# Optimization experiments

Measured on AMD Instinct MI355X. Metric: run time of the kernel, lower is better.

The kernel has to match this reference:

```python
import jax, jax.numpy as jnp
import numpy as np

B, S, D = 8, 2048, 512
H, DK, DV = 8, 64, 64


def setup_inputs() -> dict:
    key = jax.random.key(0)
    ks = jax.random.split(key, 12)
    def xavier(k, shape):
        fan_in, fan_out = shape[0], shape[1]
        std = (2.0 / (fan_in + fan_out)) ** 0.5
        return jax.random.normal(k, shape, dtype=jnp.float32) * std
    return {
        "Q": jax.random.normal(ks[0], (B, S, D), dtype=jnp.float32),
        "K": jax.random.normal(ks[1], (B, S, D), dtype=jnp.float32),
        "V": jax.random.normal(ks[2], (B, S, D), dtype=jnp.float32),
        "W_q": xavier(ks[3], (D, H * DK)),
        "W_k": xavier(ks[4], (D, H * DK)),
        "W_v": xavier(ks[5], (D, H * DV)),
        "W_o": xavier(ks[6], (H * DV, D)),
        "W1": xavier(ks[7], (D, D)),  # linear1.weight, stored [out, in]
        "b1": jnp.zeros((D,), dtype=jnp.float32),
        "W2": xavier(ks[8], (D, D)),  # linear2.weight
        "b2": jnp.zeros((D,), dtype=jnp.float32),
    }


def reference(Q, K, V, W_q, W_k, W_v, W_o, W1, b1, W2, b2):
    eps = 1e-6
    bsz, q_len, _ = Q.shape
    # project and split heads: [B, S, H, dk]
    Qh = (Q @ W_q).reshape(bsz, q_len, H, DK)
    Kh = (K @ W_k).reshape(bsz, q_len, H, DK)
    Vh = (V @ W_v).reshape(bsz, q_len, H, DV)
    temperature = DK ** 0.5
    # scores: [B, H, Sq, Sk] (full O(N^2) matrix, as in original)
    scores = jnp.einsum('bqhd,bkhd->bhqk', Qh, Kh) / (temperature + eps)
    probs = jax.nn.softmax(scores, axis=-1)  # dropout = identity (eval)
    V_att = jnp.einsum('bhqk,bkhd->bqhd', probs, Vh).reshape(bsz, q_len, H * DV)
    attn_out = V_att @ W_o  # dropout = identity
    X = Q + attn_out
    # FFN: linear2(relu(linear1(X))); torch Linear: x @ W.T + b
    ffn = jax.nn.relu(X @ W1.T + b1) @ W2.T + b2
    return ffn + X
```

## Files before the change

kernel.cpp:

```cpp
#include <hip/hip_runtime.h>
#include <stdint.h>

typedef __bf16 bf16;
typedef bf16 bf16x8 __attribute__((ext_vector_type(8)));
typedef bf16 bf16x4 __attribute__((ext_vector_type(4)));
typedef float f32x2 __attribute__((ext_vector_type(2)));
typedef float f32x4 __attribute__((ext_vector_type(4)));
typedef float f32x16 __attribute__((ext_vector_type(16)));

#define AS1 __attribute__((address_space(1)))
#define AS3 __attribute__((address_space(3)))

__device__ __forceinline__ void gll16(const void* g, void* l) {
    __builtin_amdgcn_global_load_lds((const AS1 unsigned int*)g,
                                     (AS3 unsigned int*)l, 16, 0, 0);
}

__device__ __forceinline__ bf16 f2bf(float x) { return (bf16)x; }

__device__ __forceinline__ float fexp2(float x) { return __builtin_amdgcn_exp2f(x); }

#define QSCALE_LOG2E 0.18033685757f

__global__ void k_castqkv(const float* __restrict__ Q, const float* __restrict__ K,
                          const float* __restrict__ V,
                          bf16* __restrict__ oq, bf16* __restrict__ ok, bf16* __restrict__ ov)
{
    const int z = blockIdx.y;
    const float* in = z == 0 ? Q : z == 1 ? K : V;
    bf16* out = z == 0 ? oq : z == 1 ? ok : ov;
    const int i = blockIdx.x * 256 + threadIdx.x;
    for (size_t j = (size_t)i * 4; j < 8388608u; j += (size_t)2048 * 256 * 4) {
        float4 v = *(const float4*)(in + j);
        bf16x4 o;
        o[0] = f2bf(v.x); o[1] = f2bf(v.y); o[2] = f2bf(v.z); o[3] = f2bf(v.w);
        *(bf16x4*)(out + j) = o;
    }
}

__global__ void k_castw(const float* __restrict__ Wq, const float* __restrict__ Wk,
                        const float* __restrict__ Wv, const float* __restrict__ Wo,
                        const float* __restrict__ W1, const float* __restrict__ W2,
                        bf16* __restrict__ oq, bf16* __restrict__ ok, bf16* __restrict__ ov,
                        bf16* __restrict__ oo, bf16* __restrict__ o1, bf16* __restrict__ o2)
{
    const int z = blockIdx.y;
    const int idx = blockIdx.x * 256 + threadIdx.x;
    const float* src = z == 0 ? Wq : z == 1 ? Wk : z == 2 ? Wv : z == 3 ? Wo : z == 4 ? W1 : W2;
    bf16* dst = z == 0 ? oq : z == 1 ? ok : z == 2 ? ov : z == 3 ? oo : z == 4 ? o1 : o2;
    if (z < 4) {
        const int n = idx >> 9, k = idx & 511;
        dst[idx] = f2bf(src[(k << 9) + n]);
    } else {
        dst[idx] = f2bf(src[idx]);
    }
}

__device__ __forceinline__ void gemm_core(const bf16* __restrict__ A,
                                          const bf16* __restrict__ Bt,
                                          const int K, bf16* As, bf16* Bs,
                                          const int bm, const int bn,
                                          f32x4 acc[4][4])
{
    const int tid  = threadIdx.x;
    const int lane = tid & 63;
    const int wave = tid >> 6;
    const int g    = lane >> 4;
    const int l15  = lane & 15;
    const int wm   = (wave >> 1) * 64;
    const int wn   = (wave & 1) * 64;

    const int srow = tid >> 2;
    const int sk   = (tid & 3) * 8;
    const size_t aoff0 = (size_t)(bm + srow) * K + sk;
    const size_t aoff1 = (size_t)(bm + 64 + srow) * K + sk;
    const size_t boff0 = (size_t)(bn + srow) * K + sk;
    const size_t boff1 = (size_t)(bn + 64 + srow) * K + sk;
    char* asb = (char*)As + wave * 1024;
    char* bsb = (char*)Bs + wave * 1024;

    for (int kt = 0; kt < K; kt += 32) {
        __syncthreads();
        gll16(A + aoff0 + kt, asb);
        gll16(A + aoff1 + kt, asb + 4096);
        gll16(Bt + boff0 + kt, bsb);
        gll16(Bt + boff1 + kt, bsb + 4096);
        __syncthreads();
        bf16x8 af[4], bfv[4];
#pragma unroll
        for (int mi = 0; mi < 4; ++mi)
            af[mi] = *(const bf16x8*)&As[(wm + mi * 16 + l15) * 32 + g * 8];
#pragma unroll
        for (int ni = 0; ni < 4; ++ni)
            bfv[ni] = *(const bf16x8*)&Bs[(wn + ni * 16 + l15) * 32 + g * 8];
#pragma unroll
        for (int mi = 0; mi < 4; ++mi)
#pragma unroll
            for (int ni = 0; ni < 4; ++ni)
                acc[mi][ni] = __builtin_amdgcn_mfma_f32_16x16x32_bf16(
                    af[mi], bfv[ni], acc[mi][ni], 0, 0, 0);
    }
}

template<int EPI>
__global__ __launch_bounds__(256)
void k_gemm(const bf16* __restrict__ A, const bf16* __restrict__ Bt,
            const float* __restrict__ bias,
            const bf16* __restrict__ residb,
            float* __restrict__ Cf, bf16* __restrict__ Cb,
            int M, int N, int K)
{
    __shared__ bf16 As[128 * 32];
    __shared__ bf16 Bs[128 * 32];
    const int bm = blockIdx.y * 128, bn = blockIdx.x * 128;
    f32x4 acc[4][4] = {};
    gemm_core(A, Bt, K, As, Bs, bm, bn, acc);

    const int tid  = threadIdx.x;
    const int lane = tid & 63;
    const int wave = tid >> 6;
    const int g    = lane >> 4;
    const int l15  = lane & 15;
    const int wm   = (wave >> 1) * 64;
    const int wn   = (wave & 1) * 64;
    const int col0 = bn + wn + l15;
#pragma unroll
    for (int ni = 0; ni < 4; ++ni) {
        const int col = col0 + ni * 16;
        float bv = 0.f;
        if constexpr (EPI == 2 || EPI == 3) bv = bias[col];
#pragma unroll
        for (int mi = 0; mi < 4; ++mi) {
#pragma unroll
            for (int r = 0; r < 4; ++r) {
                const int row = bm + wm + mi * 16 + 4 * g + r;
                const size_t idx = (size_t)row * N + col;
                float v = acc[mi][ni][r];
                if constexpr (EPI == 1) {
                    Cb[idx] = f2bf(v + (float)residb[idx]);
                } else if constexpr (EPI == 2) {
                    Cb[idx] = f2bf(fmaxf(v + bv, 0.f));
                } else {
                    Cf[idx] = v + bv + (float)residb[idx];
                }
            }
        }
    }
}

__global__ __launch_bounds__(256)
void k_proj(const bf16* __restrict__ Qb, const bf16* __restrict__ Kb, const bf16* __restrict__ Vb,
            const bf16* __restrict__ BQ, const bf16* __restrict__ BK, const bf16* __restrict__ BV,
            bf16* __restrict__ OQ, bf16* __restrict__ OK_, bf16* __restrict__ OV)
{
    __shared__ bf16 SM[8192];
    const int z = blockIdx.z;
    const bf16* A  = z == 0 ? Qb : z == 1 ? Kb : Vb;
    const bf16* Bt = z == 0 ? BQ : z == 1 ? BK : BV;
    bf16* Cb       = z == 0 ? OQ : z == 1 ? OK_ : OV;
    const int bm = blockIdx.y * 128, bn = blockIdx.x * 128;
    f32x4 acc[4][4] = {};
    gemm_core(A, Bt, 512, SM, SM + 4096, bm, bn, acc);

    const int tid  = threadIdx.x;
    const int lane = tid & 63;
    const int wave = tid >> 6;
    const int g    = lane >> 4;
    const int l15  = lane & 15;
    const int wn   = (wave & 1) * 64;
    const int bb   = bm >> 11;
    const int s0   = bm & 2047;

    __syncthreads();
#pragma unroll
    for (int p = 0; p < 2; ++p) {
        if ((wave >> 1) == p) {
            if (z == 0) {
#pragma unroll
                for (int ni = 0; ni < 4; ++ni) {
                    const int col = wn + ni * 16 + l15;
                    const int hh = col >> 6, dk = col & 63;
                    char* img = (char*)SM + hh * 8192;
#pragma unroll
                    for (int mi = 0; mi < 4; ++mi)
#pragma unroll
                        for (int r = 0; r < 4; ++r) {
                            const int sl = mi * 16 + 4 * g + r;
                            *(bf16*)(img + (sl * 64 + dk) * 2) =
                                f2bf(acc[mi][ni][r] * QSCALE_LOG2E);
                        }
                }
            } else if (z == 1) {
#pragma unroll
                for (int ni = 0; ni < 4; ++ni) {
                    const int col = wn + ni * 16 + l15;
                    const int hh = col >> 6, dk = col & 63;
                    const int ks = dk >> 4, h2 = (dk >> 3) & 1, e = dk & 7;
                    char* img = (char*)SM + hh * 8192;
#pragma unroll
                    for (int mi = 0; mi < 4; ++mi)
#pragma unroll
                        for (int r = 0; r < 4; ++r) {
                            const int sl = mi * 16 + 4 * g + r;
                            const int t2 = sl >> 5, ql = sl & 31;
                            const int off = (((t2 * 4 + ks) * 64 + h2 * 32 + ql) * 8 + e) * 2;
                            *(bf16*)(img + off) = f2bf(acc[mi][ni][r]);
                        }
                }
            } else {
#pragma unroll
                for (int ni = 0; ni < 4; ++ni) {
                    const int col = wn + ni * 16 + l15;
                    const int hh = col >> 6, dv = col & 63;
                    const int dvt = dv >> 5, ql = dv & 31;
                    char* img = (char*)SM + hh * 8192;
#pragma unroll
                    for (int mi = 0; mi < 4; ++mi)
#pragma unroll
                        for (int r = 0; r < 4; ++r) {
                            const int sl = mi * 16 + 4 * g + r;
                            const int kt = sl >> 4, kk = sl & 15;
                            const int h2 = (kk >> 2) & 1;
                            const int e = (kk & 3) | ((kk >> 3) << 2);
                            const int off = (((dvt * 4 + kt) * 64 + h2 * 32 + ql) * 8 + e) * 2;
                            *(bf16*)(img + off) = f2bf(acc[mi][ni][r]);
                        }
                }
            }
        }
        __syncthreads();
        {
            const int hh = tid >> 7, t = tid & 127;
            const int hg = (bn >> 6) + hh;
            const size_t a0 = (size_t)(bb * 8 + hg) * 131072;
            const size_t slab = (z == 0) ? a0 + (size_t)(s0 + p * 64) * 64
                                         : a0 + (size_t)((s0 >> 6) + p) * 4096;
            const char* img = (const char*)SM + hh * 8192;
#pragma unroll
            for (int i = 0; i < 4; ++i) {
                const int G = i * 128 + t;
                bf16x8 vv = *(const bf16x8*)(img + G * 16);
                *(bf16x8*)&Cb[slab + (size_t)G * 8] = vv;
            }
        }
        if (p == 0) __syncthreads();
    }
}

__global__ __launch_bounds__(256, 2)
void k_attn(const bf16* __restrict__ Qp, const bf16* __restrict__ Khp,
            const bf16* __restrict__ Vtp, bf16* __restrict__ O)
{
    __shared__ bf16 smem[16384];
    const int tid = threadIdx.x;
    const int l   = tid & 63;
    const int w   = tid >> 6;
    const int h   = l >> 5;
    const int ql  = l & 31;
    const int d   = blockIdx.x;
    const int bh  = ((d >> 6) << 3) | (d & 7);
    const int qt  = (d >> 3) & 7;
    const size_t base = (size_t)bh * 131072;
    const int q0 = qt * 256 + w * 64;
    const int loff = l * 16;

    bf16x8 qfA[4], qfB[4];
#pragma unroll
    for (int ks = 0; ks < 4; ++ks) {
        qfA[ks] = *(const bf16x8*)&Qp[base + (size_t)(q0 + ql) * 64 + ks * 16 + h * 8];
        qfB[ks] = *(const bf16x8*)&Qp[base + (size_t)(q0 + 32 + ql) * 64 + ks * 16 + h * 8];
    }

    f32x16 oA0 = {}, oA1 = {}, oB0 = {}, oB1 = {};
    float lrunA = 0.f, lrunB = 0.f;

    const bf16* ksrc = Khp + base + tid * 8;
    const bf16* vsrc = Vtp + base + tid * 8;
    char* kb0 = (char*)smem;
    char* kb1 = (char*)smem + 16384;
    const int wdst = w * 1024;

    auto stage = [&](int kvt, char* kb) {
        const bf16* ks = ksrc + kvt * 4096;
        const bf16* vs = vsrc + kvt * 4096;
        gll16(ks,        kb + wdst);
        gll16(ks + 2048, kb + 4096 + wdst);
        gll16(vs,        kb + 8192 + wdst);
        gll16(vs + 2048, kb + 12288 + wdst);
    };

    auto compute = [&](const char* kb) {
        f32x16 sA0 = {}, sA1 = {}, sB0 = {}, sB1 = {};
        __builtin_amdgcn_s_setprio(1);
#pragma unroll
        for (int ks = 0; ks < 4; ++ks) {
            bf16x8 a0 = *(const bf16x8*)(kb + ks * 1024 + loff);
            bf16x8 a1 = *(const bf16x8*)(kb + 4096 + ks * 1024 + loff);
            sA0 = __builtin_amdgcn_mfma_f32_32x32x16_bf16(a0, qfA[ks], sA0, 0, 0, 0);
            sB0 = __builtin_amdgcn_mfma_f32_32x32x16_bf16(a0, qfB[ks], sB0, 0, 0, 0);
            sA1 = __builtin_amdgcn_mfma_f32_32x32x16_bf16(a1, qfA[ks], sA1, 0, 0, 0);
            sB1 = __builtin_amdgcn_mfma_f32_32x32x16_bf16(a1, qfB[ks], sB1, 0, 0, 0);
        }
        __builtin_amdgcn_s_setprio(0);

        f32x2 pA = {0.f, 0.f}, pB = {0.f, 0.f};
#pragma unroll
        for (int r = 0; r < 16; r += 2) {
            sA0[r]     = fexp2(sA0[r]);
            sA0[r + 1] = fexp2(sA0[r + 1]);
            sA1[r]     = fexp2(sA1[r]);
            sA1[r + 1] = fexp2(sA1[r + 1]);
            pA += (f32x2){sA0[r], sA0[r + 1]};
            pA += (f32x2){sA1[r], sA1[r + 1]};
        }
#pragma unroll
        for (int r = 0; r < 16; r += 2) {
            sB0[r]     = fexp2(sB0[r]);
            sB0[r + 1] = fexp2(sB0[r + 1]);
            sB1[r]     = fexp2(sB1[r]);
            sB1[r + 1] = fexp2(sB1[r + 1]);
            pB += (f32x2){sB0[r], sB0[r + 1]};
            pB += (f32x2){sB1[r], sB1[r + 1]};
        }
        lrunA += pA[0] + pA[1];
        lrunB += pB[0] + pB[1];

        bf16x8 pbA[4], pbB[4];
#pragma unroll
        for (int j = 0; j < 4; ++j) {
            const int ofs = 8 * (j & 1);
#pragma unroll
            for (int e = 0; e < 8; ++e) {
                pbA[j][e] = f2bf((j & 2) ? sA1[ofs + e] : sA0[ofs + e]);
                pbB[j][e] = f2bf((j & 2) ? sB1[ofs + e] : sB0[ofs + e]);
            }
        }

        const char* vr = kb + 8192;
        __builtin_amdgcn_s_setprio(1);
#pragma unroll
        for (int j = 0; j < 4; ++j) {
            bf16x8 a0 = *(const bf16x8*)(vr + j * 1024 + loff);
            bf16x8 a1 = *(const bf16x8*)(vr + 4096 + j * 1024 + loff);
            oA0 = __builtin_amdgcn_mfma_f32_32x32x16_bf16(a0, pbA[j], oA0, 0, 0, 0);
            oB0 = __builtin_amdgcn_mfma_f32_32x32x16_bf16(a0, pbB[j], oB0, 0, 0, 0);
            oA1 = __builtin_amdgcn_mfma_f32_32x32x16_bf16(a1, pbA[j], oA1, 0, 0, 0);
            oB1 = __builtin_amdgcn_mfma_f32_32x32x16_bf16(a1, pbB[j], oB1, 0, 0, 0);
        }
        __builtin_amdgcn_s_setprio(0);
    };

    stage(0, kb0);
    __syncthreads();
    for (int kvt = 0; kvt < 32; kvt += 2) {
        if (kvt + 1 < 32) stage(kvt + 1, kb1);
        compute(kb0);
        __syncthreads();
        if (kvt + 2 < 32) stage(kvt + 2, kb0);
        compute(kb1);
        __syncthreads();
    }

    char* ot = (char*)smem + w * 4096;
    const int qr = l >> 1;
    const int dh4 = (l & 1) * 4;
    auto epi = [&](const f32x16& e0, const f32x16& e1, float lr, int qg) {
        lr += __shfl_xor(lr, 32);
        const float inv = 1.f / lr;
#pragma unroll
        for (int dvt = 0; dvt < 2; ++dvt) {
#pragma unroll
            for (int r = 0; r < 16; ++r) {
                const int dv = dvt * 32 + (r & 3) + 8 * (r >> 2) + 4 * h;
                const float val = (dvt ? e1[r] : e0[r]) * inv;
                *(bf16*)(ot + ql * 128 + ((((dv >> 3) ^ (ql & 7)) << 4) | ((dv & 7) << 1))) = f2bf(val);
            }
        }
        const size_t ob = ((size_t)(bh >> 3) * 2048 + qg + qr) * 512 + (bh & 7) * 64 + (size_t)dh4 * 8;
#pragma unroll
        for (int B = 0; B < 4; ++B) {
            bf16x8 v = *(const bf16x8*)(ot + qr * 128 + (((dh4 + B) ^ (qr & 7)) << 4));
            *(bf16x8*)&O[ob + B * 8] = v;
        }
    };
    epi(oA0, oA1, lrunA, q0);
    epi(oB0, oB1, lrunB, q0 + 32);
}

extern "C" void kernel_launch(void* const* d_in, const int* in_sizes, int n_in,
                              void* d_out, int out_size, void* d_ws, size_t ws_size,
                              hipStream_t stream)
{
    const float* Q  = (const float*)d_in[0];
    const float* K  = (const float*)d_in[1];
    const float* V  = (const float*)d_in[2];
    const float* Wq = (const float*)d_in[3];
    const float* Wk = (const float*)d_in[4];
    const float* Wv = (const float*)d_in[5];
    const float* Wo = (const float*)d_in[6];
    const float* W1 = (const float*)d_in[7];
    const float* b1 = (const float*)d_in[8];
    const float* W2 = (const float*)d_in[9];
    const float* b2 = (const float*)d_in[10];
    float* out = (float*)d_out;

    const int M = 8 * 2048;
    const size_t TN = (size_t)M * 512;
    const int WN = 512 * 512;

    char* ws = (char*)d_ws;
    bf16* Qbf  = (bf16*)ws;
    bf16* Kbf  = Qbf + TN;
    bf16* Vbf  = Kbf + TN;
    bf16* Qhp  = Vbf + TN;
    bf16* Khp  = Qhp + TN;
    bf16* Vtp  = Khp + TN;
    bf16* Vatt = Vtp + TN;
    bf16* H1   = Vatt + TN;
    bf16* Wqt  = H1 + TN;
    bf16* Wkt  = Wqt + WN;
    bf16* Wvt  = Wkt + WN;
    bf16* Wot  = Wvt + WN;
    bf16* W1b  = Wot + WN;
    bf16* W2b  = W1b + WN;
    bf16* Xbf  = Vbf;

    k_castqkv<<<dim3(2048, 3), 256, 0, stream>>>(Q, K, V, Qbf, Kbf, Vbf);
    k_castw<<<dim3(1024, 6), 256, 0, stream>>>(Wq, Wk, Wv, Wo, W1, W2,
                                               Wqt, Wkt, Wvt, Wot, W1b, W2b);

    k_proj<<<dim3(4, 128, 3), 256, 0, stream>>>(Qbf, Kbf, Vbf, Wqt, Wkt, Wvt,
                                                Qhp, Khp, Vtp);

    k_attn<<<512, 256, 0, stream>>>(Qhp, Khp, Vtp, Vatt);

    dim3 gg(4, 128);
    k_gemm<1><<<gg, 256, 0, stream>>>(Vatt, Wot, nullptr, Qbf, nullptr, Xbf, M, 512, 512);
    k_gemm<2><<<gg, 256, 0, stream>>>(Xbf, W1b, b1, nullptr, nullptr, H1, M, 512, 512);
    k_gemm<3><<<gg, 256, 0, stream>>>(H1, W2b, b2, Xbf, out, nullptr, M, 512, 512);
}
```

Baseline: 210.2 us.

## Drop pre-tiled QKV projection layouts; attention reads natural row-major and transposed V

The projection kernel no longer stages its output through LDS into MFMA-ready tiled images. It writes Q and K row-major (Q pre-scaled) and V transposed per head directly from registers. The attention kernel now gathers K and V tiles from these natural layouts, using an XOR swizzle on the V staging and split 8-byte LDS reads. The residual for the first output GEMM now comes from the fp32 Q input instead of its bf16 copy, which also changes accuracy slightly. This removes the projection epilogue's LDS round trip and barriers, at the cost of strided scalar/4-wide global stores and less contiguous attention loads.

```diff
diff --git a/kernel.cpp b/kernel.cpp
--- a/kernel.cpp
+++ b/kernel.cpp
@@ -105,7 +105,7 @@
 template<int EPI>
 __global__ __launch_bounds__(256)
 void k_gemm(const bf16* __restrict__ A, const bf16* __restrict__ Bt,
-            const float* __restrict__ bias,
+            const float* __restrict__ bias, const float* __restrict__ residf,
             const bf16* __restrict__ residb,
             float* __restrict__ Cf, bf16* __restrict__ Cb,
             int M, int N, int K)
@@ -137,7 +137,7 @@
                 const size_t idx = (size_t)row * N + col;
                 float v = acc[mi][ni][r];
                 if constexpr (EPI == 1) {
-                    Cb[idx] = f2bf(v + (float)residb[idx]);
+                    Cb[idx] = f2bf(v + residf[idx]);
                 } else if constexpr (EPI == 2) {
                     Cb[idx] = f2bf(fmaxf(v + bv, 0.f));
                 } else {
@@ -153,103 +153,55 @@
             const bf16* __restrict__ BQ, const bf16* __restrict__ BK, const bf16* __restrict__ BV,
             bf16* __restrict__ OQ, bf16* __restrict__ OK_, bf16* __restrict__ OV)
 {
-    __shared__ bf16 SM[8192];
+    __shared__ bf16 As[128 * 32];
+    __shared__ bf16 Bs[128 * 32];
     const int z = blockIdx.z;
     const bf16* A  = z == 0 ? Qb : z == 1 ? Kb : Vb;
     const bf16* Bt = z == 0 ? BQ : z == 1 ? BK : BV;
     bf16* Cb       = z == 0 ? OQ : z == 1 ? OK_ : OV;
     const int bm = blockIdx.y * 128, bn = blockIdx.x * 128;
     f32x4 acc[4][4] = {};
-    gemm_core(A, Bt, 512, SM, SM + 4096, bm, bn, acc);
+    gemm_core(A, Bt, 512, As, Bs, bm, bn, acc);
 
     const int tid  = threadIdx.x;
     const int lane = tid & 63;
     const int wave = tid >> 6;
     const int g    = lane >> 4;
     const int l15  = lane & 15;
+    const int wm   = (wave >> 1) * 64;
     const int wn   = (wave & 1) * 64;
-    const int bb   = bm >> 11;
-    const int s0   = bm & 2047;
-
-    __syncthreads();
-#pragma unroll
-    for (int p = 0; p < 2; ++p) {
-        if ((wave >> 1) == p) {
-            if (z == 0) {
-#pragma unroll
-                for (int ni = 0; ni < 4; ++ni) {
-                    const int col = wn + ni * 16 + l15;
-                    const int hh = col >> 6, dk = col & 63;
-                    char* img = (char*)SM + hh * 8192;
-#pragma unroll
-                    for (int mi = 0; mi < 4; ++mi)
-#pragma unroll
-                        for (int r = 0; r < 4; ++r) {
-                            const int sl = mi * 16 + 4 * g + r;
-                            *(bf16*)(img + (sl * 64 + dk) * 2) =
-                                f2bf(acc[mi][ni][r] * QSCALE_LOG2E);
-                        }
+    const int col0 = bn + wn + l15;
+#pragma unroll
+    for (int ni = 0; ni < 4; ++ni) {
+        const int col = col0 + ni * 16;
+        if (z < 2) {
+            const float sc = (z == 0) ? QSCALE_LOG2E : 1.f;
+#pragma unroll
+            for (int mi = 0; mi < 4; ++mi)
+#pragma unroll
+                for (int r = 0; r < 4; ++r) {
+                    const int row = bm + wm + mi * 16 + 4 * g + r;
+                    Cb[(size_t)row * 512 + col] = f2bf(acc[mi][ni][r] * sc);
                 }
-            } else if (z == 1) {
-#pragma unroll
-                for (int ni = 0; ni < 4; ++ni) {
-                    const int col = wn + ni * 16 + l15;
-                    const int hh = col >> 6, dk = col & 63;
-                    const int ks = dk >> 4, h2 = (dk >> 3) & 1, e = dk & 7;
-                    char* img = (char*)SM + hh * 8192;
-#pragma unroll
-                    for (int mi = 0; mi < 4; ++mi)
-#pragma unroll
-                        for (int r = 0; r < 4; ++r) {
-                            const int sl = mi * 16 + 4 * g + r;
-                            const int t2 = sl >> 5, ql = sl & 31;
-                            const int off = (((t2 * 4 + ks) * 64 + h2 * 32 + ql) * 8 + e) * 2;
-                            *(bf16*)(img + off) = f2bf(acc[mi][ni][r]);
-                        }
-                }
-            } else {
-#pragma unroll
-                for (int ni = 0; ni < 4; ++ni) {
-                    const int col = wn + ni * 16 + l15;
-                    const int hh = col >> 6, dv = col & 63;
-                    const int dvt = dv >> 5, ql = dv & 31;
-                    char* img = (char*)SM + hh * 8192;
-#pragma unroll
-                    for (int mi = 0; mi < 4; ++mi)
-#pragma unroll
-                        for (int r = 0; r < 4; ++r) {
-                            const int sl = mi * 16 + 4 * g + r;
-                            const int kt = sl >> 4, kk = sl & 15;
-                            const int h2 = (kk >> 2) & 1;
-                            const int e = (kk & 3) | ((kk >> 3) << 2);
-                            const int off = (((dvt * 4 + kt) * 64 + h2 * 32 + ql) * 8 + e) * 2;
-                            *(bf16*)(img + off) = f2bf(acc[mi][ni][r]);
-                        }
-                }
+        } else {
+            const int hcol = col >> 6, dv = col & 63;
+#pragma unroll
+            for (int mi = 0; mi < 4; ++mi) {
+                const int row = bm + wm + mi * 16 + 4 * g;
+                const int b2 = row >> 11, sl = row & 2047;
+                const size_t addr = ((size_t)(b2 * 8 + hcol) * 64 + dv) * 2048 + sl;
+                bf16x4 vv;
+#pragma unroll
+                for (int r = 0; r < 4; ++r) vv[r] = f2bf(acc[mi][ni][r]);
+                *(bf16x4*)&Cb[addr] = vv;
             }
         }
-        __syncthreads();
-        {
-            const int hh = tid >> 7, t = tid & 127;
-            const int hg = (bn >> 6) + hh;
-            const size_t a0 = (size_t)(bb * 8 + hg) * 131072;
-            const size_t slab = (z == 0) ? a0 + (size_t)(s0 + p * 64) * 64
-                                         : a0 + (size_t)((s0 >> 6) + p) * 4096;
-            const char* img = (const char*)SM + hh * 8192;
-#pragma unroll
-            for (int i = 0; i < 4; ++i) {
-                const int G = i * 128 + t;
-                bf16x8 vv = *(const bf16x8*)(img + G * 16);
-                *(bf16x8*)&Cb[slab + (size_t)G * 8] = vv;
-            }
-        }
-        if (p == 0) __syncthreads();
     }
 }
 
 __global__ __launch_bounds__(256, 2)
-void k_attn(const bf16* __restrict__ Qp, const bf16* __restrict__ Khp,
-            const bf16* __restrict__ Vtp, bf16* __restrict__ O)
+void k_attn(const bf16* __restrict__ Qn, const bf16* __restrict__ Kn,
+            const bf16* __restrict__ Vt, bf16* __restrict__ O)
 {
     __shared__ bf16 smem[16384];
     const int tid = threadIdx.x;
@@ -260,33 +212,39 @@
     const int d   = blockIdx.x;
     const int bh  = ((d >> 6) << 3) | (d & 7);
     const int qt  = (d >> 3) & 7;
-    const size_t base = (size_t)bh * 131072;
+    const int b   = bh >> 3, head = bh & 7;
     const int q0 = qt * 256 + w * 64;
     const int loff = l * 16;
 
     bf16x8 qfA[4], qfB[4];
-#pragma unroll
-    for (int ks = 0; ks < 4; ++ks) {
-        qfA[ks] = *(const bf16x8*)&Qp[base + (size_t)(q0 + ql) * 64 + ks * 16 + h * 8];
-        qfB[ks] = *(const bf16x8*)&Qp[base + (size_t)(q0 + 32 + ql) * 64 + ks * 16 + h * 8];
+    {
+        const size_t qrow = (size_t)(b * 2048 + q0 + ql) * 512 + head * 64;
+#pragma unroll
+        for (int ks = 0; ks < 4; ++ks) {
+            qfA[ks] = *(const bf16x8*)&Qn[qrow + ks * 16 + h * 8];
+            qfB[ks] = *(const bf16x8*)&Qn[qrow + (size_t)32 * 512 + ks * 16 + h * 8];
+        }
     }
 
     f32x16 oA0 = {}, oA1 = {}, oB0 = {}, oB1 = {};
     float lrunA = 0.f, lrunB = 0.f;
 
-    const bf16* ksrc = Khp + base + tid * 8;
-    const bf16* vsrc = Vtp + base + tid * 8;
+    const int ks2 = tid >> 6, h2k = (tid >> 5) & 1, qlk = tid & 31;
+    const bf16* ksrc = Kn + (size_t)(b * 2048 + qlk) * 512 + head * 64 + ks2 * 16 + h2k * 8;
+    const int dv1 = tid >> 3;
+    const bf16* vsrc = Vt + ((size_t)bh * 64 + dv1) * 2048 + (((tid & 7) ^ (dv1 & 7)) << 3);
+
     char* kb0 = (char*)smem;
     char* kb1 = (char*)smem + 16384;
     const int wdst = w * 1024;
 
     auto stage = [&](int kvt, char* kb) {
-        const bf16* ks = ksrc + kvt * 4096;
-        const bf16* vs = vsrc + kvt * 4096;
-        gll16(ks,        kb + wdst);
-        gll16(ks + 2048, kb + 4096 + wdst);
-        gll16(vs,        kb + 8192 + wdst);
-        gll16(vs + 2048, kb + 12288 + wdst);
+        const bf16* ks = ksrc + (size_t)kvt * 64 * 512;
+        const bf16* vs = vsrc + kvt * 64;
+        gll16(ks,                      kb + wdst);
+        gll16(ks + (size_t)32 * 512,   kb + 4096 + wdst);
+        gll16(vs,                      kb + 8192 + wdst);
+        gll16(vs + (size_t)32 * 2048,  kb + 12288 + wdst);
     };
 
     auto compute = [&](const char* kb) {
@@ -337,15 +295,22 @@
         }
 
         const char* vr = kb + 8192;
+        const int sw = ql & 7;
         __builtin_amdgcn_s_setprio(1);
 #pragma unroll
         for (int j = 0; j < 4; ++j) {
-            bf16x8 a0 = *(const bf16x8*)(vr + j * 1024 + loff);
-            bf16x8 a1 = *(const bf16x8*)(vr + 4096 + j * 1024 + loff);
-            oA0 = __builtin_amdgcn_mfma_f32_32x32x16_bf16(a0, pbA[j], oA0, 0, 0, 0);
-            oB0 = __builtin_amdgcn_mfma_f32_32x32x16_bf16(a0, pbB[j], oB0, 0, 0, 0);
-            oA1 = __builtin_amdgcn_mfma_f32_32x32x16_bf16(a1, pbA[j], oA1, 0, 0, 0);
-            oB1 = __builtin_amdgcn_mfma_f32_32x32x16_bf16(a1, pbB[j], oB1, 0, 0, 0);
+            union U8 { struct { bf16x4 lo, hi; } p; bf16x8 v; };
+            U8 u0, u1;
+            const int ga = (((2 * j)     ^ sw) << 4) + 8 * h;
+            const int gb = (((2 * j + 1) ^ sw) << 4) + 8 * h;
+            u0.p.lo = *(const bf16x4*)(vr + ql * 128 + ga);
+            u0.p.hi = *(const bf16x4*)(vr + ql * 128 + gb);
+            u1.p.lo = *(const bf16x4*)(vr + 4096 + ql * 128 + ga);
+            u1.p.hi = *(const bf16x4*)(vr + 4096 + ql * 128 + gb);
+            oA0 = __builtin_amdgcn_mfma_f32_32x32x16_bf16(u0.v, pbA[j], oA0, 0, 0, 0);
+            oB0 = __builtin_amdgcn_mfma_f32_32x32x16_bf16(u0.v, pbB[j], oB0, 0, 0, 0);
+            oA1 = __builtin_amdgcn_mfma_f32_32x32x16_bf16(u1.v, pbA[j], oA1, 0, 0, 0);
+            oB1 = __builtin_amdgcn_mfma_f32_32x32x16_bf16(u1.v, pbB[j], oB1, 0, 0, 0);
         }
         __builtin_amdgcn_s_setprio(0);
     };
@@ -376,7 +341,7 @@
                 *(bf16*)(ot + ql * 128 + ((((dv >> 3) ^ (ql & 7)) << 4) | ((dv & 7) << 1))) = f2bf(val);
             }
         }
-        const size_t ob = ((size_t)(bh >> 3) * 2048 + qg + qr) * 512 + (bh & 7) * 64 + (size_t)dh4 * 8;
+        const size_t ob = ((size_t)b * 2048 + qg + qr) * 512 + head * 64 + (size_t)dh4 * 8;
 #pragma unroll
         for (int B = 0; B < 4; ++B) {
             bf16x8 v = *(const bf16x8*)(ot + qr * 128 + (((dh4 + B) ^ (qr & 7)) << 4));
@@ -412,10 +377,10 @@
     bf16* Qbf  = (bf16*)ws;
     bf16* Kbf  = Qbf + TN;
     bf16* Vbf  = Kbf + TN;
-    bf16* Qhp  = Vbf + TN;
-    bf16* Khp  = Qhp + TN;
-    bf16* Vtp  = Khp + TN;
-    bf16* Vatt = Vtp + TN;
+    bf16* Qpn  = Vbf + TN;
+    bf16* Kpn  = Qpn + TN;
+    bf16* Vtn  = Kpn + TN;
+    bf16* Vatt = Vtn + TN;
     bf16* H1   = Vatt + TN;
     bf16* Wqt  = H1 + TN;
     bf16* Wkt  = Wqt + WN;
@@ -423,19 +388,19 @@
     bf16* Wot  = Wvt + WN;
     bf16* W1b  = Wot + WN;
     bf16* W2b  = W1b + WN;
-    bf16* Xbf  = Vbf;
+    bf16* Xbf  = Qbf;
 
     k_castqkv<<<dim3(2048, 3), 256, 0, stream>>>(Q, K, V, Qbf, Kbf, Vbf);
     k_castw<<<dim3(1024, 6), 256, 0, stream>>>(Wq, Wk, Wv, Wo, W1, W2,
                                                Wqt, Wkt, Wvt, Wot, W1b, W2b);
 
     k_proj<<<dim3(4, 128, 3), 256, 0, stream>>>(Qbf, Kbf, Vbf, Wqt, Wkt, Wvt,
-                                                Qhp, Khp, Vtp);
-
-    k_attn<<<512, 256, 0, stream>>>(Qhp, Khp, Vtp, Vatt);
+                                                Qpn, Kpn, Vtn);
+
+    k_attn<<<512, 256, 0, stream>>>(Qpn, Kpn, Vtn, Vatt);
 
     dim3 gg(4, 128);
-    k_gemm<1><<<gg, 256, 0, stream>>>(Vatt, Wot, nullptr, Qbf, nullptr, Xbf, M, 512, 512);
-    k_gemm<2><<<gg, 256, 0, stream>>>(Xbf, W1b, b1, nullptr, nullptr, H1, M, 512, 512);
-    k_gemm<3><<<gg, 256, 0, stream>>>(H1, W2b, b2, Xbf, out, nullptr, M, 512, 512);
-}
+    k_gemm<1><<<gg, 256, 0, stream>>>(Vatt, Wot, nullptr, Q, nullptr, nullptr, Xbf, M, 512, 512);
+    k_gemm<2><<<gg, 256, 0, stream>>>(Xbf, W1b, b1, nullptr, nullptr, nullptr, H1, M, 512, 512);
+    k_gemm<3><<<gg, 256, 0, stream>>>(H1, W2b, b2, nullptr, Xbf, out, nullptr, M, 512, 512);
+}
```

Result: slower. 218.1 us (+3.8%).
